# Kernel optimization log

Hardware: AMD Instinct MI355X
Metric: run time of the kernel (lower is better)

Reference implementation:

```python
import jax, jax.numpy as jnp
import numpy as np

B, DIM, L, H, W = 4, 128, 256, 8, 8
N = L * H * W
D_INNER, D_STATE, D_CONV, DT_RANK = 128, 8, 4, 8


def _ln(x, w, b, eps=1e-5):
    m = x.mean(-1, keepdims=True)
    v = ((x - m) ** 2).mean(-1, keepdims=True)
    return (x - m) * jax.lax.rsqrt(v + eps) * w + b


def _mamba_fusion(x, z_in, p, i):
    # x, z_in: (B, N, DIM). x drives the SSM; z_in provides the cross-modal gate.
    u = x @ p['Wx'][i]                                    # (B, N, D_INNER)
    z = z_in @ p['Wz'][i]                                 # (B, N, D_INNER)
    # causal depthwise conv1d along tokens, kernel D_CONV (torch pad=k-1 then truncate)
    up = jnp.pad(u, ((0, 0), (D_CONV - 1, 0), (0, 0)))
    w = p['conv_w'][i]                                    # (D_INNER, D_CONV)
    uc = sum(up[:, k:k + u.shape[1], :] * w[:, k] for k in range(D_CONV)) + p['conv_b'][i]
    uc = jax.nn.silu(uc)
    x_dbl = uc @ p['Wxproj'][i]                           # (B, N, DT_RANK + 2*D_STATE)
    dt_r, Bm, Cm = jnp.split(x_dbl, [DT_RANK, DT_RANK + D_STATE], axis=-1)
    dt = jax.nn.softplus(dt_r @ p['Wdt'][i] + p['bdt'][i])  # (B, N, D_INNER)
    A = -jnp.exp(p['A_log'][i])                           # (D_INNER, D_STATE)
    dA = jnp.exp(dt[..., None] * A)                       # (B, N, D_INNER, D_STATE)
    dBu = dt[..., None] * Bm[:, :, None, :] * uc[..., None]

    def step(h, inp):
        dA_t, dBu_t, C_t = inp
        h = dA_t * h + dBu_t                              # (B, D_INNER, D_STATE)
        return h, jnp.einsum('bds,bs->bd', h, C_t)

    h0 = jnp.zeros((u.shape[0], D_INNER, D_STATE), u.dtype)
    _, ys = jax.lax.scan(step, h0, (dA.swapaxes(0, 1), dBu.swapaxes(0, 1), Cm.swapaxes(0, 1)))
    y = ys.swapaxes(0, 1) + p['Dp'][i] * uc
    y = y * jax.nn.silu(z)
    return y @ p['Wout_m'][i] + p['bout_m'][i]


def _cross_block(in0, in1, p, i):
    skip = in0
    a = _ln(in0, p['ln0_w'][i], p['ln0_b'][i])
    b = _ln(in1, p['ln1_w'][i], p['ln1_b'][i])
    return skip + _mamba_fusion(a, b, p, i)


def setup_inputs() -> dict:
    key = jax.random.key(0)
    ks = jax.random.split(key, 16)
    s_in = 1.0 / np.sqrt(DIM)
    s_di = 1.0 / np.sqrt(D_INNER)
    inp = {
        'front': jax.random.normal(ks[0], (B, DIM, L, H, W), jnp.float32),
        'back': jax.random.normal(ks[1], (B, DIM, L, H, W), jnp.float32),
        'ln0_w': jnp.ones((2, DIM), jnp.float32),
        'ln0_b': jnp.zeros((2, DIM), jnp.float32),
        'ln1_w': jnp.ones((2, DIM), jnp.float32),
        'ln1_b': jnp.zeros((2, DIM), jnp.float32),
        'Wx': jax.random.normal(ks[2], (2, DIM, D_INNER), jnp.float32) * s_in,
        'Wz': jax.random.normal(ks[3], (2, DIM, D_INNER), jnp.float32) * s_in,
        'conv_w': jax.random.normal(ks[4], (2, D_INNER, D_CONV), jnp.float32) * 0.5,
        'conv_b': jnp.zeros((2, D_INNER), jnp.float32),
        'Wxproj': jax.random.normal(ks[5], (2, D_INNER, DT_RANK + 2 * D_STATE), jnp.float32) * s_di,
        'Wdt': jax.random.normal(ks[6], (2, DT_RANK, D_INNER), jnp.float32) * (1.0 / np.sqrt(DT_RANK)),
        'bdt': jnp.full((2, D_INNER), -4.6, jnp.float32),  # softplus^-1(~0.01)
        'A_log': jnp.broadcast_to(jnp.log(jnp.arange(1, D_STATE + 1, dtype=jnp.float32)), (2, D_INNER, D_STATE)).copy(),
        'Dp': jnp.ones((2, D_INNER), jnp.float32),
        'Wout_m': jax.random.normal(ks[7], (2, D_INNER, DIM), jnp.float32) * s_di,
        'bout_m': jnp.zeros((2, DIM), jnp.float32),
        'Wout': jax.random.normal(ks[8], (DIM, DIM), jnp.float32) * s_in,
        'bout': jnp.zeros((DIM,), jnp.float32),
    }
    return inp


def reference(front, back, ln0_w, ln0_b, ln1_w, ln1_b, Wx, Wz, conv_w, conv_b,
              Wxproj, Wdt, bdt, A_log, Dp, Wout_m, bout_m, Wout, bout):
    p = dict(ln0_w=ln0_w, ln0_b=ln0_b, ln1_w=ln1_w, ln1_b=ln1_b, Wx=Wx, Wz=Wz,
             conv_w=conv_w, conv_b=conv_b, Wxproj=Wxproj, Wdt=Wdt, bdt=bdt,
             A_log=A_log, Dp=Dp, Wout_m=Wout_m, bout_m=bout_m)
    ff = front.reshape(B, DIM, N).swapaxes(1, 2)          # (B, N, DIM)
    bf = back.reshape(B, DIM, N).swapaxes(1, 2)
    f_fus = _cross_block(ff, bf, p, 0)
    b_fus = _cross_block(bf, ff, p, 1)
    fusion = ((f_fus + b_fus) * 0.5) @ Wout + bout
    return fusion.swapaxes(1, 2).reshape(B, DIM, L, H, W)
```

## Files before the change

### kernel.cpp

```cpp
#include <hip/hip_runtime.h>

#define DEV static __device__ __forceinline__

typedef short s16x8 __attribute__((ext_vector_type(8)));
typedef float f32x4 __attribute__((ext_vector_type(4)));
typedef unsigned short u16;
typedef unsigned int u32;

DEV float b2f(u16 u){ return __uint_as_float(((unsigned int)u) << 16); }
DEV u16 f2b(float f){
  unsigned int x = __float_as_uint(f);
  x += 0x7fffu + ((x >> 16) & 1u);
  return (u16)(x >> 16);
}
DEV float silu_f(float x){ return x * __builtin_amdgcn_rcpf(1.f + __expf(-x)); }
DEV float softplus_f(float x){ return (x > 15.f) ? x : __logf(1.f + __expf(x)); }
DEV bool detf32(const void* lnw){ return *(const unsigned int*)lnw == 0x3F800000u; }
DEV float ldin(const void* p, long long i, bool f){
  return f ? ((const float*)p)[i] : b2f(((const u16*)p)[i]);
}

static constexpr int BATCH = 4;
static constexpr int NSEQ  = 16384;
static constexpr int RTOT  = BATCH * NSEQ;
static constexpr int GCH   = 256;
static constexpr int DIRSZ = BATCH*GCH*128*8;

DEV int swz(int row, int col){ return (row << 7) + (col ^ ((row & 7) << 3)); }

__global__ __launch_bounds__(256) void k_setup(
                        const void* ln0w, const void* ln0b, const void* ln1w, const void* ln1b,
                        const void* Wx, const void* Wz, const void* Wxp, const void* Wdt,
                        const void* bdt, const void* Alog, const void* convw, const void* convb,
                        const void* Dpr, const void* Woutm, const void* boutm,
                        const void* Wout, const void* bout,
                        u16* Wuz, u16* WdtBC, u16* Wcat, u16* WoutT,
                        float* buz, float* bdtf, float* bcat, float* boutf,
                        float* Aexp, float* convwF, float* convbF, float* DpF)
{
  bool f = detf32(ln0w);
  int tid = blockIdx.x * 256 + threadIdx.x;
  int gs  = gridDim.x * 256;
  for (int idx = tid; idx < 2*256*128; idx += gs){
    int d = idx >> 15; int n = (idx >> 7) & 255; int k = idx & 127;
    float wv;
    if (n < 128) wv = ldin(ln0w, d*128+k, f) * ldin(Wx, (long long)(d*128+k)*128 + n, f);
    else         wv = ldin(ln1w, (1-d)*128+k, f) * ldin(Wz, (long long)((1-d)*128+k)*128 + (n-128), f);
    Wuz[idx] = f2b(wv);
  }
  for (int idx = tid; idx < 2*256; idx += gs){
    int d = idx >> 8; int n = idx & 255;
    float s = 0.f;
    if (n < 128){
      for (int k = 0; k < 128; ++k)
        s += ldin(ln0b, d*128+k, f) * ldin(Wx, (long long)(d*128+k)*128 + n, f);
    } else {
      for (int k = 0; k < 128; ++k)
        s += ldin(ln1b, (1-d)*128+k, f) * ldin(Wz, (long long)((1-d)*128+k)*128 + (n-128), f);
    }
    buz[idx] = s;
  }
  for (int idx = tid; idx < 2*128; idx += gs)
    bdtf[idx] = ldin(bdt, idx, f);
  for (int idx = tid; idx < 2*144*128; idx += gs){
    int i = idx / (144*128); int rem = idx % (144*128); int n = rem >> 7; int k = rem & 127;
    if (n < 128){
      float s = 0.f;
      for (int j = 0; j < 8; ++j)
        s += ldin(Wxp, (long long)(i*128+k)*24 + j, f) * ldin(Wdt, (long long)(i*8+j)*128 + n, f);
      WdtBC[idx] = f2b(s);
    } else {
      WdtBC[idx] = f2b(ldin(Wxp, (long long)(i*128+k)*24 + (n - 120), f));
    }
  }
  for (int idx = tid; idx < 128*256; idx += gs){
    int n = idx >> 8; int k = idx & 255;
    Wcat[idx] = f2b(ldin(Woutm, (long long)k*128 + n, f));
  }
  for (int idx = tid; idx < 128*128; idx += gs){
    int n = idx >> 7, k = idx & 127;
    WoutT[idx] = f2b(ldin(Wout, (long long)k*128 + n, f));
  }
  for (int idx = tid; idx < 128; idx += gs){
    bcat[idx]  = ldin(boutm, idx, f) + ldin(boutm, 128 + idx, f);
    boutf[idx] = ldin(bout, idx, f);
  }
  for (int idx = tid; idx < 2*128*8; idx += gs)
    Aexp[idx] = -expf(ldin(Alog, idx, f));
  for (int idx = tid; idx < 2*128*4; idx += gs)
    convwF[idx] = ldin(convw, idx, f);
  for (int idx = tid; idx < 2*128; idx += gs){
    convbF[idx] = ldin(convb, idx, f);
    DpF[idx]   = ldin(Dpr, idx, f);
  }
}

__global__ __launch_bounds__(256, 3) void k_lnguz(const void* front, const void* back,
                                                  const void* ln0w,
                                                  const u16* __restrict__ Wuz,
                                                  const float* __restrict__ buz,
                                                  u16* __restrict__ sfbh,
                                                  u16* __restrict__ u0, u16* __restrict__ u1,
                                                  u16* __restrict__ z0, u16* __restrict__ z1)
{
  bool fF = detf32(ln0w);
  __shared__ u16 Tf[64][130];
  __shared__ u16 Tb[64][130];
  __shared__ __align__(16) u16 Wl[64*128];
  __shared__ float Mf[64], Rf[64], Mb[64], Rb[64];
  int tid = threadIdx.x;
  long long r0 = (long long)blockIdx.x * 64;
  int b  = (int)(r0 >> 14);
  int n0 = (int)(r0 & 16383);
  if (fF){
    const float* fp = (const float*)front;
    const float* bp = (const float*)back;
    for (int it = 0; it < 8; ++it){
      int d = it*16 + (tid >> 4);
      int t = (tid & 15) * 4;
      long long gi = ((long long)(b*128 + d))*NSEQ + n0 + t;
      float4 vf = *(const float4*)&fp[gi];
      float4 vb = *(const float4*)&bp[gi];
      Tf[t+0][d] = f2b(vf.x); Tf[t+1][d] = f2b(vf.y);
      Tf[t+2][d] = f2b(vf.z); Tf[t+3][d] = f2b(vf.w);
      Tb[t+0][d] = f2b(vb.x); Tb[t+1][d] = f2b(vb.y);
      Tb[t+2][d] = f2b(vb.z); Tb[t+3][d] = f2b(vb.w);
    }
  } else {
    const u16* fp = (const u16*)front;
    const u16* bp = (const u16*)back;
    for (int it = 0; it < 4; ++it){
      int d = it*32 + (tid >> 3);
      int t = (tid & 7) * 8;
      long long gi = ((long long)(b*128 + d))*NSEQ + n0 + t;
      uint4 vf = *(const uint4*)&fp[gi];
      uint4 vb = *(const uint4*)&bp[gi];
      Tf[t+0][d] = (u16)vf.x; Tf[t+1][d] = (u16)(vf.x>>16);
      Tf[t+2][d] = (u16)vf.y; Tf[t+3][d] = (u16)(vf.y>>16);
      Tf[t+4][d] = (u16)vf.z; Tf[t+5][d] = (u16)(vf.z>>16);
      Tf[t+6][d] = (u16)vf.w; Tf[t+7][d] = (u16)(vf.w>>16);
      Tb[t+0][d] = (u16)vb.x; Tb[t+1][d] = (u16)(vb.x>>16);
      Tb[t+2][d] = (u16)vb.y; Tb[t+3][d] = (u16)(vb.y>>16);
      Tb[t+4][d] = (u16)vb.z; Tb[t+5][d] = (u16)(vb.z>>16);
      Tb[t+6][d] = (u16)vb.w; Tb[t+7][d] = (u16)(vb.w>>16);
    }
  }
  __syncthreads();
  {
    int t = tid >> 2, sub = tid & 3;
    float s = 0.f, ss = 0.f, s2 = 0.f, ss2 = 0.f;
    for (int k = 0; k < 32; ++k){
      float v = b2f(Tf[t][sub*32 + k]); s  += v; ss  += v*v;
      float w = b2f(Tb[t][sub*32 + k]); s2 += w; ss2 += w*w;
    }
    for (int m = 1; m < 4; m <<= 1){
      s  += __shfl_xor(s,  m, 64); ss  += __shfl_xor(ss,  m, 64);
      s2 += __shfl_xor(s2, m, 64); ss2 += __shfl_xor(ss2, m, 64);
    }
    if (sub == 0){
      float mf = s  * (1.f/128.f); float vf = ss  * (1.f/128.f) - mf*mf;
      Mf[t] = mf; Rf[t] = rsqrtf(vf + 1e-5f);
      float mb = s2 * (1.f/128.f); float vb = ss2 * (1.f/128.f) - mb*mb;
      Mb[t] = mb; Rb[t] = rsqrtf(vb + 1e-5f);
    }
  }
  __syncthreads();
  for (int it = 0; it < 8; ++it){
    int t = it*8 + (tid >> 5);
    int c = (tid & 31) * 4;
    float mf = Mf[t], rf = Rf[t], mb = Mb[t], rb = Rb[t];
    float f0 = b2f(Tf[t][c+0]), f1 = b2f(Tf[t][c+1]), f2 = b2f(Tf[t][c+2]), f3 = b2f(Tf[t][c+3]);
    float g0 = b2f(Tb[t][c+0]), g1 = b2f(Tb[t][c+1]), g2 = b2f(Tb[t][c+2]), g3 = b2f(Tb[t][c+3]);
    ushort4 so;
    so.x = f2b(f0+g0); so.y = f2b(f1+g1); so.z = f2b(f2+g2); so.w = f2b(f3+g3);
    *(ushort4*)&sfbh[(r0 + t)*128 + c] = so;
    Tf[t][c+0] = f2b((f0-mf)*rf); Tf[t][c+1] = f2b((f1-mf)*rf);
    Tf[t][c+2] = f2b((f2-mf)*rf); Tf[t][c+3] = f2b((f3-mf)*rf);
    Tb[t][c+0] = f2b((g0-mb)*rb); Tb[t][c+1] = f2b((g1-mb)*rb);
    Tb[t][c+2] = f2b((g2-mb)*rb); Tb[t][c+3] = f2b((g3-mb)*rb);
  }
  __syncthreads();
  int w = tid >> 6, lane = tid & 63;
  int q = lane >> 4, m = lane & 15;
  for (int dir = 0; dir < 2; ++dir){
    const u16* At = dir ? &Tb[0][0] : &Tf[0][0];
    const u16* Wt = Wuz + dir*256*128;
    const float* bias = buz + dir*256;
    u16* outU = dir ? u1 : u0;
    u16* outZ = dir ? z0 : z1;
    for (int ch = 0; ch < 4; ++ch){
      for (int ci = tid; ci < 64*16; ci += 256){
        int n = ci >> 4, c8 = ci & 15;
        *(uint4*)&Wl[(n << 7) + ((c8 ^ (n & 7)) << 3)] = *(const uint4*)&Wt[(ch*64 + n)*128 + c8*8];
      }
      __syncthreads();
      f32x4 acc[4];
      #pragma unroll
      for (int ct = 0; ct < 4; ++ct) acc[ct] = (f32x4){0.f,0.f,0.f,0.f};
      #pragma unroll
      for (int kt = 0; kt < 4; ++kt){
        const u16* ap = At + (w*16 + m)*130 + kt*32 + q*8;
        union { u32 w4[4]; s16x8 v; } au;
        au.w4[0] = *(const u32*)&ap[0];
        au.w4[1] = *(const u32*)&ap[2];
        au.w4[2] = *(const u32*)&ap[4];
        au.w4[3] = *(const u32*)&ap[6];
        int sc = (kt*32 + q*8) ^ ((m & 7) << 3);
        #pragma unroll
        for (int ct = 0; ct < 4; ++ct){
          s16x8 bf = *(const s16x8*)&Wl[((ct*16 + m) << 7) + sc];
          acc[ct] = __builtin_amdgcn_mfma_f32_16x16x32_bf16(au.v, bf, acc[ct], 0, 0, 0);
        }
      }
      #pragma unroll
      for (int ct = 0; ct < 4; ++ct){
        int col = ch*64 + ct*16 + m;
        #pragma unroll
        for (int i = 0; i < 4; ++i){
          long long r = r0 + w*16 + q*4 + i;
          float v = acc[ct][i] + bias[col];
          if (col < 128) outU[r*128 + col] = f2b(v);
          else           outZ[r*128 + (col - 128)] = f2b(silu_f(v));
        }
      }
      __syncthreads();
    }
  }
}

__global__ __launch_bounds__(256, 3) void k_cps(const u16* __restrict__ u0p,
                                             const u16* __restrict__ u1p,
                                             const float* __restrict__ convwF,
                                             const float* __restrict__ convbF,
                                             const u16* __restrict__ WdtBC,
                                             const float* __restrict__ bdtf,
                                             const float* __restrict__ Aexp,
                                             u16* __restrict__ uc0p, u16* __restrict__ uc1p,
                                             u16* __restrict__ yg,
                                             float* __restrict__ BCg,
                                             float* __restrict__ P, float* __restrict__ Q)
{
  __shared__ __align__(16) u16 AlF[64*128];
  __shared__ __align__(16) u16 WlF[144*128];
  int dir = blockIdx.y;
  const u16* u = dir ? u1p : u0p;
  u16* ucb = dir ? uc1p : uc0p;
  const u16* Wt = WdtBC + dir*18432;
  const float* bias = bdtf + dir*128;
  u16* dtb = yg + dir*128;
  float* BC = BCg + (long long)dir*RTOT*16;
  int tid = threadIdx.x;
  long long r0 = (long long)blockIdx.x * 64;
  int b  = (int)(r0 >> 14);
  int n0 = (int)(r0 & 16383);
  for (int ci = tid; ci < 144*16; ci += 256){
    int n = ci >> 4, c8 = ci & 15;
    *(uint4*)&WlF[(n << 7) + ((c8 ^ (n & 7)) << 3)] = *(const uint4*)&Wt[n*128 + c8*8];
  }
  {
    int c = tid & 127, h = tid >> 7;
    const float* wp = &convwF[(dir*128 + c)*4];
    float w0 = wp[0], w1 = wp[1], w2 = wp[2], w3 = wp[3];
    float cb = convbF[dir*128 + c];
    int t0 = h*32;
    const u16* up = u + (long long)b*NSEQ*128 + c;
    int nbase = n0 + t0;
    float win0 = (nbase-3 >= 0) ? b2f(up[(long long)(nbase-3)*128]) : 0.f;
    float win1 = (nbase-2 >= 0) ? b2f(up[(long long)(nbase-2)*128]) : 0.f;
    float win2 = (nbase-1 >= 0) ? b2f(up[(long long)(nbase-1)*128]) : 0.f;
    #pragma unroll
    for (int t = 0; t < 32; ++t){
      float cur = b2f(up[(long long)(nbase + t)*128]);
      float a = win0*w0 + win1*w1 + win2*w2 + cur*w3 + cb;
      u16 s = f2b(silu_f(a));
      AlF[swz(t0 + t, c)] = s;
      ucb[(r0 + t0 + t)*128 + c] = s;
      win0 = win1; win1 = win2; win2 = cur;
    }
  }
  __syncthreads();
  int w = tid >> 6, lane = tid & 63;
  int q = lane >> 4, m = lane & 15;
  f32x4 acc[9];
  #pragma unroll
  for (int ct = 0; ct < 9; ++ct) acc[ct] = (f32x4){0.f,0.f,0.f,0.f};
  #pragma unroll
  for (int kt = 0; kt < 4; ++kt){
    int sc = (kt*32 + q*8) ^ ((m & 7) << 3);
    s16x8 af = *(const s16x8*)&AlF[((w*16 + m) << 7) + sc];
    #pragma unroll
    for (int ct = 0; ct < 9; ++ct){
      s16x8 bf = *(const s16x8*)&WlF[((ct*16 + m) << 7) + sc];
      acc[ct] = __builtin_amdgcn_mfma_f32_16x16x32_bf16(af, bf, acc[ct], 0, 0, 0);
    }
  }
  __syncthreads();
  u16* Dl = WlF;
  float* BCl = (float*)&WlF[64*128];
  #pragma unroll
  for (int ct = 0; ct < 9; ++ct){
    int col = ct*16 + m;
    #pragma unroll
    for (int i = 0; i < 4; ++i){
      int rl = w*16 + q*4 + i;
      long long r = r0 + rl;
      float v = acc[ct][i];
      if (col < 128){
        u16 dv = f2b(softplus_f(v + bias[col]));
        dtb[r*256 + col] = dv;
        Dl[swz(rl, col)] = dv;
      } else {
        BC[r*16 + (col - 128)] = v;
        BCl[rl*16 + (col - 128)] = v;
      }
    }
  }
  __syncthreads();
  {
    int c = tid & 127, sh = tid >> 7;
    int g = (int)(r0 & 16383) >> 6;
    int base = sh*4;
    float Ac[4], Pr[4], H[4];
    bool fast = true;
    #pragma unroll
    for (int j = 0; j < 4; ++j){
      Ac[j] = Aexp[(dir*128 + c)*8 + base + j];
      fast = fast && (fabsf(Ac[j] + (float)(base + j + 1)) < 2e-4f);
      H[j] = 0.f;
    }
    float sd = 0.f;
    if (fast){
      if (sh == 0){
        for (int t = 0; t < 64; ++t){
          int ce = swz(t, c);
          float d  = b2f(Dl[ce]);
          float uu = b2f(AlF[ce]);
          float du = d * uu;
          sd += d;
          float E  = __expf(-d);
          float E2 = E*E, E3 = E2*E, E4 = E2*E2;
          float4 bc = *(const float4*)&BCl[t*16];
          H[0] = E *H[0] + du*bc.x;
          H[1] = E2*H[1] + du*bc.y;
          H[2] = E3*H[2] + du*bc.z;
          H[3] = E4*H[3] + du*bc.w;
        }
        float Es = __expf(-sd);
        Pr[0] = Es; Pr[1] = Es*Es; Pr[2] = Pr[1]*Es; Pr[3] = Pr[1]*Pr[1];
      } else {
        for (int t = 0; t < 64; ++t){
          int ce = swz(t, c);
          float d  = b2f(Dl[ce]);
          float uu = b2f(AlF[ce]);
          float du = d * uu;
          sd += d;
          float E  = __expf(-d);
          float E2 = E*E, E4 = E2*E2;
          float E5 = E4*E, E6 = E5*E, E7 = E6*E, E8 = E7*E;
          float4 bc = *(const float4*)&BCl[t*16 + 4];
          H[0] = E5*H[0] + du*bc.x;
          H[1] = E6*H[1] + du*bc.y;
          H[2] = E7*H[2] + du*bc.z;
          H[3] = E8*H[3] + du*bc.w;
        }
        float Es = __expf(-sd);
        float Es2 = Es*Es, Es4 = Es2*Es2;
        Pr[0] = Es4*Es; Pr[1] = Es4*Es2; Pr[2] = Pr[1]*Es; Pr[3] = Es4*Es4;
      }
    } else {
      for (int t = 0; t < 64; ++t){
        int ce = swz(t, c);
        float d  = b2f(Dl[ce]);
        float uu = b2f(AlF[ce]);
        float du = d * uu;
        sd += d;
        #pragma unroll
        for (int j = 0; j < 4; ++j){
          float dA = __expf(d * Ac[j]);
          H[j]  = dA*H[j] + du*BCl[t*16 + base + j];
        }
      }
      #pragma unroll
      for (int j = 0; j < 4; ++j) Pr[j] = __expf(sd * Ac[j]);
    }
    long long o = (long long)dir*DIRSZ + (((long long)b*GCH + g)*128 + c)*8 + base;
    *(float4*)&P[o] = make_float4(Pr[0],Pr[1],Pr[2],Pr[3]);
    *(float4*)&Q[o] = make_float4(H[0],H[1],H[2],H[3]);
  }
}

__global__ __launch_bounds__(64) void k_scan2(const float* __restrict__ P,
                                              const float* __restrict__ Q,
                                              float* __restrict__ hinit)
{
  int idx = blockIdx.x*64 + threadIdx.x;
  int dir = idx >> 12;
  int rem = idx & 4095;
  int b  = rem >> 10;
  int cs = rem & 1023;
  long long base = (long long)dir*DIRSZ + (long long)b*GCH*1024 + cs;
  float h = 0.f;
  for (int g = 0; g < GCH; g += 8){
    long long o = base + (long long)g*1024;
    float p[8], qv[8];
    #pragma unroll
    for (int j = 0; j < 8; ++j){ p[j] = P[o + j*1024]; qv[j] = Q[o + j*1024]; }
    #pragma unroll
    for (int j = 0; j < 8; ++j){
      hinit[o + j*1024] = h;
      h = p[j]*h + qv[j];
    }
  }
}

__global__ __launch_bounds__(256) void k_scan3(const u16* __restrict__ uc0p,
                                               const u16* __restrict__ uc1p,
                                               const float* __restrict__ BCg,
                                               const float* __restrict__ hinit,
                                               const u16* __restrict__ z0p,
                                               const u16* __restrict__ z1p,
                                               const float* __restrict__ DpF,
                                               const float* __restrict__ Aexp,
                                               u16* yg)
{
  __shared__ float Bl[128][8];
  __shared__ float Cl[128][8];
  int dir = blockIdx.y;
  const u16* uc = dir ? uc1p : uc0p;
  const u16* zs = dir ? z1p : z0p;
  const float* BC = BCg + (long long)dir*RTOT*16;
  int tid = threadIdx.x;
  int gp = blockIdx.x & 127;
  int b  = blockIdx.x >> 7;
  long long tokbase = (long long)b*NSEQ + gp*128;
  for (int idx = tid; idx < 128*8; idx += 256){
    int row = idx >> 3, s = idx & 7;
    Bl[row][s] = BC[(tokbase + row)*16 + s];
    Cl[row][s] = BC[(tokbase + row)*16 + 8 + s];
  }
  __syncthreads();
  int c = tid & 127;
  int gh = tid >> 7;
  int g = gp*2 + gh;
  int doff = dir*128;
  float Ac[8], H[8];
  long long ho = (long long)dir*DIRSZ + (((long long)b*GCH + g)*128 + c)*8;
  float4 h0 = *(const float4*)&hinit[ho];
  float4 h1 = *(const float4*)&hinit[ho + 4];
  H[0]=h0.x; H[1]=h0.y; H[2]=h0.z; H[3]=h0.w;
  H[4]=h1.x; H[5]=h1.y; H[6]=h1.z; H[7]=h1.w;
  bool fast = true;
  #pragma unroll
  for (int s = 0; s < 8; ++s){
    Ac[s] = Aexp[(dir*128 + c)*8 + s];
    fast = fast && (fabsf(Ac[s] + (float)(s + 1)) < 2e-4f);
  }
  float dpc = DpF[dir*128 + c];
  long long rbase = (long long)b*NSEQ + g*64;
  if (fast){
    for (int t = 0; t < 64; ++t){
      long long r = rbase + t;
      float d  = b2f(yg[r*256 + doff + c]);
      float uu = b2f(uc[r*128 + c]);
      float du = d * uu;
      int rowl = gh*64 + t;
      float E  = __expf(-d);
      float E2 = E*E, E3 = E2*E, E4 = E2*E2;
      float dA[8] = {E, E2, E3, E4, E4*E, E4*E2, E4*E3, E4*E4};
      float y = 0.f;
      #pragma unroll
      for (int s = 0; s < 8; ++s){
        H[s] = dA[s]*H[s] + du*Bl[rowl][s];
        y += H[s]*Cl[rowl][s];
      }
      float zv = b2f(zs[r*128 + c]);
      yg[r*256 + doff + c] = f2b((y + dpc*uu) * zv);
    }
  } else {
    for (int t = 0; t < 64; ++t){
      long long r = rbase + t;
      float d  = b2f(yg[r*256 + doff + c]);
      float uu = b2f(uc[r*128 + c]);
      float du = d * uu;
      int rowl = gh*64 + t;
      float y = 0.f;
      #pragma unroll
      for (int s = 0; s < 8; ++s){
        float dA = __expf(d * Ac[s]);
        H[s] = dA*H[s] + du*Bl[rowl][s];
        y += H[s]*Cl[rowl][s];
      }
      float zv = b2f(zs[r*128 + c]);
      yg[r*256 + doff + c] = f2b((y + dpc*uu) * zv);
    }
  }
}

__global__ __launch_bounds__(256, 3) void k_tail(const u16* __restrict__ yg,
                                              const u16* __restrict__ Wcat,
                                              const float* __restrict__ bcat,
                                              const u16* __restrict__ sfbh,
                                              const u16* __restrict__ WoutT,
                                              const float* __restrict__ boutf,
                                              void* outp, const void* dflag)
{
  __shared__ u16 Wl[128][136];
  __shared__ u16 Al[64][136];
  int tid = threadIdx.x;
  long long r0 = (long long)blockIdx.x * 64;
  int w = tid >> 6, lane = tid & 63;
  int q = lane >> 4, m = lane & 15;
  f32x4 acc[8];
  #pragma unroll
  for (int ct = 0; ct < 8; ++ct) acc[ct] = (f32x4){0.f,0.f,0.f,0.f};
  for (int kp = 0; kp < 2; ++kp){
    if (kp) __syncthreads();
    for (int ci = tid; ci < 128*16; ci += 256){
      int n = ci >> 4, c8 = ci & 15;
      *(uint4*)&Wl[n][c8*8] = *(const uint4*)&Wcat[n*256 + kp*128 + c8*8];
    }
    for (int ci = tid; ci < 64*16; ci += 256){
      int rl = ci >> 4, c8 = ci & 15;
      *(uint4*)&Al[rl][c8*8] = *(const uint4*)&yg[(r0 + rl)*256 + kp*128 + c8*8];
    }
    __syncthreads();
    #pragma unroll
    for (int kt = 0; kt < 4; ++kt){
      s16x8 af = *(const s16x8*)&Al[w*16 + m][kt*32 + q*8];
      #pragma unroll
      for (int ct = 0; ct < 8; ++ct){
        s16x8 bf = *(const s16x8*)&Wl[ct*16 + m][kt*32 + q*8];
        acc[ct] = __builtin_amdgcn_mfma_f32_16x16x32_bf16(af, bf, acc[ct], 0, 0, 0);
      }
    }
  }
  __syncthreads();
  #pragma unroll
  for (int ct = 0; ct < 8; ++ct){
    int col = ct*16 + m;
    #pragma unroll
    for (int i = 0; i < 4; ++i){
      int rl = w*16 + q*4 + i;
      long long r = r0 + rl;
      Al[rl][col] = f2b(acc[ct][i] + bcat[col] + b2f(sfbh[r*128 + col]));
    }
  }
  for (int ci = tid; ci < 128*16; ci += 256){
    int n = ci >> 4, c8 = ci & 15;
    *(uint4*)&Wl[n][c8*8] = *(const uint4*)&WoutT[n*128 + c8*8];
  }
  __syncthreads();
  f32x4 acc2[8];
  #pragma unroll
  for (int ct = 0; ct < 8; ++ct) acc2[ct] = (f32x4){0.f,0.f,0.f,0.f};
  #pragma unroll
  for (int kt = 0; kt < 4; ++kt){
    s16x8 af = *(const s16x8*)&Al[w*16 + m][kt*32 + q*8];
    #pragma unroll
    for (int ct = 0; ct < 8; ++ct){
      s16x8 bf = *(const s16x8*)&Wl[ct*16 + m][kt*32 + q*8];
      acc2[ct] = __builtin_amdgcn_mfma_f32_16x16x32_bf16(af, bf, acc2[ct], 0, 0, 0);
    }
  }
  __syncthreads();
  u16* Tl = &Wl[0][0];
  #pragma unroll
  for (int ct = 0; ct < 8; ++ct){
    int col = ct*16 + m;
    #pragma unroll
    for (int i = 0; i < 4; ++i){
      int rl = w*16 + q*4 + i;
      Tl[col*68 + rl] = f2b(0.5f*acc2[ct][i] + boutf[col]);
    }
  }
  __syncthreads();
  long long b = r0 >> 14; long long tok0 = r0 & 16383;
  bool fo = detf32(dflag);
  if (fo){
    float* of = (float*)outp;
    for (int idx = tid; idx < 128*16; idx += 256){
      int n = idx >> 4; int t0 = (idx & 15)*4;
      float4 v;
      v.x = b2f(Tl[n*68 + t0+0]); v.y = b2f(Tl[n*68 + t0+1]);
      v.z = b2f(Tl[n*68 + t0+2]); v.w = b2f(Tl[n*68 + t0+3]);
      *(float4*)&of[(((long long)(b*128 + n)) << 14) + tok0 + t0] = v;
    }
  } else {
    u16* ob = (u16*)outp;
    for (int idx = tid; idx < 128*16; idx += 256){
      int n = idx >> 4; int t0 = (idx & 15)*4;
      ushort4 v;
      v.x = Tl[n*68 + t0+0]; v.y = Tl[n*68 + t0+1];
      v.z = Tl[n*68 + t0+2]; v.w = Tl[n*68 + t0+3];
      *(ushort4*)&ob[(((long long)(b*128 + n)) << 14) + tok0 + t0] = v;
    }
  }
}

extern "C" void kernel_launch(void* const* d_in, const int* in_sizes, int n_in,
                              void* d_out, int out_size, void* d_ws, size_t ws_size,
                              hipStream_t stream)
{
  (void)in_sizes; (void)n_in; (void)out_size; (void)ws_size;
  const void* front = d_in[0];
  const void* back  = d_in[1];
  const void* ln0w  = d_in[2];
  const void* ln0b  = d_in[3];
  const void* ln1w  = d_in[4];
  const void* ln1b  = d_in[5];
  const void* Wx    = d_in[6];
  const void* Wz    = d_in[7];
  const void* convw = d_in[8];
  const void* convb = d_in[9];
  const void* Wxp   = d_in[10];
  const void* Wdt   = d_in[11];
  const void* bdt   = d_in[12];
  const void* Alog  = d_in[13];
  const void* Dpr   = d_in[14];
  const void* Woutm = d_in[15];
  const void* boutm = d_in[16];
  const void* Wout  = d_in[17];
  const void* bout  = d_in[18];

  char* p = (char*)d_ws;
  auto alloc = [&](size_t bytes) -> void* {
    void* q = (void*)p; p += (bytes + 255) & ~(size_t)255; return q;
  };
  u16*   uc0   = (u16*)  alloc((size_t)RTOT*128*2);
  u16*   uc1   = (u16*)  alloc((size_t)RTOT*128*2);
  u16*   sfbh  = (u16*)  alloc((size_t)RTOT*128*2);
  u16*   u0    = (u16*)  alloc((size_t)RTOT*128*2);
  u16*   u1    = (u16*)  alloc((size_t)RTOT*128*2);
  u16*   z0    = (u16*)  alloc((size_t)RTOT*128*2);
  u16*   z1    = (u16*)  alloc((size_t)RTOT*128*2);
  float* BC    = (float*)alloc((size_t)2*RTOT*16*4);
  float* Pb    = (float*)alloc((size_t)2*DIRSZ*4);
  float* Qb    = (float*)alloc((size_t)2*DIRSZ*4);
  float* hin   = (float*)alloc((size_t)2*DIRSZ*4);
  u16*   yg    = (u16*)  alloc((size_t)RTOT*256*2);
  u16*   Wuz   = (u16*)  alloc(2*256*128*2);
  u16*   WdtBC = (u16*)  alloc(2*144*128*2);
  u16*   Wcat  = (u16*)  alloc(128*256*2);
  u16*   WoutT = (u16*)  alloc(128*128*2);
  float* buz   = (float*)alloc(2*256*4);
  float* bdtf  = (float*)alloc(2*128*4);
  float* bcat  = (float*)alloc(128*4);
  float* boutf = (float*)alloc(128*4);
  float* Aexp  = (float*)alloc(2*128*8*4);
  float* convwF= (float*)alloc(2*128*4*4);
  float* convbF= (float*)alloc(2*128*4);
  float* DpF   = (float*)alloc(2*128*4);

  k_setup<<<128,256,0,stream>>>(ln0w,ln0b,ln1w,ln1b,Wx,Wz,Wxp,Wdt,bdt,Alog,convw,convb,Dpr,
                                Woutm,boutm,Wout,bout,
                                Wuz,WdtBC,Wcat,WoutT,buz,bdtf,bcat,boutf,Aexp,
                                convwF,convbF,DpF);
  k_lnguz<<<RTOT/64,256,0,stream>>>(front, back, ln0w, Wuz, buz, sfbh,
                                    u0, u1, z0, z1);
  dim3 g2(RTOT/64, 2);
  k_cps<<<g2,256,0,stream>>>(u0, u1, convwF, convbF, WdtBC, bdtf, Aexp,
                             uc0, uc1, yg, BC, Pb, Qb);
  k_scan2<<<128,64,0,stream>>>(Pb, Qb, hin);
  dim3 g3(BATCH*GCH/2, 2);
  k_scan3<<<g3,256,0,stream>>>(uc0, uc1, BC, hin, z0, z1, DpF, Aexp, yg);
  k_tail<<<RTOT/64,256,0,stream>>>(yg, Wcat, bcat, sfbh, WoutT, boutf, d_out, ln0w);
}
```

Measured before the change: 312.1 us.

## Register-prefetch weight tiles to overlap global loads with MFMA in GEMM kernels

In the LN+projection kernel and the tail kernel, the next weight (and activation) tile is now loaded from global memory into registers before the current tile's MFMA work runs, so load latency overlaps with compute. The LN kernel also hoists the A-fragment loads out of the chunk loop and drops one barrier per iteration. The scan kernel batches eight timesteps' global loads ahead of the recurrence so memory latency is less serialized. This costs more registers per thread, which may reduce occupancy under the launch bounds.

Result: slower. 359.8 us (+15.3%).

```diff
diff --git a/kernel.cpp b/kernel.cpp
--- a/kernel.cpp
+++ b/kernel.cpp
@@ -112,6 +112,7 @@
   long long r0 = (long long)blockIdx.x * 64;
   int b  = (int)(r0 >> 14);
   int n0 = (int)(r0 & 16383);
+  int pn = tid >> 4, pc8 = tid & 15;
   if (fF){
     const float* fp = (const float*)front;
     const float* bp = (const float*)back;
@@ -145,6 +146,10 @@
       Tb[t+6][d] = (u16)vb.w; Tb[t+7][d] = (u16)(vb.w>>16);
     }
   }
+  uint4 wreg[4];
+  #pragma unroll
+  for (int k = 0; k < 4; ++k)
+    wreg[k] = *(const uint4*)&Wuz[(pn + 16*k)*128 + pc8*8];
   __syncthreads();
   {
     int t = tid >> 2, sub = tid & 3;
@@ -182,21 +187,22 @@
   __syncthreads();
   int w = tid >> 6, lane = tid & 63;
   int q = lane >> 4, m = lane & 15;
-  for (int dir = 0; dir < 2; ++dir){
-    const u16* At = dir ? &Tb[0][0] : &Tf[0][0];
-    const u16* Wt = Wuz + dir*256*128;
-    const float* bias = buz + dir*256;
-    u16* outU = dir ? u1 : u0;
-    u16* outZ = dir ? z0 : z1;
-    for (int ch = 0; ch < 4; ++ch){
-      for (int ci = tid; ci < 64*16; ci += 256){
-        int n = ci >> 4, c8 = ci & 15;
-        *(uint4*)&Wl[(n << 7) + ((c8 ^ (n & 7)) << 3)] = *(const uint4*)&Wt[(ch*64 + n)*128 + c8*8];
-      }
-      __syncthreads();
-      f32x4 acc[4];
+  s16x8 afr[4];
+  for (int rd = 0; rd < 8; ++rd){
+    int dir = rd >> 2;
+    #pragma unroll
+    for (int k = 0; k < 4; ++k)
+      *(uint4*)&Wl[((pn + 16*k) << 7) + ((pc8 ^ (pn & 7)) << 3)] = wreg[k];
+    __syncthreads();
+    if (rd < 7){
+      int nd = (rd+1) >> 2, nc = (rd+1) & 3;
+      const u16* Wt = Wuz + nd*256*128;
       #pragma unroll
-      for (int ct = 0; ct < 4; ++ct) acc[ct] = (f32x4){0.f,0.f,0.f,0.f};
+      for (int k = 0; k < 4; ++k)
+        wreg[k] = *(const uint4*)&Wt[(nc*64 + pn + 16*k)*128 + pc8*8];
+    }
+    if ((rd & 3) == 0){
+      const u16* At = dir ? &Tb[0][0] : &Tf[0][0];
       #pragma unroll
       for (int kt = 0; kt < 4; ++kt){
         const u16* ap = At + (w*16 + m)*130 + kt*32 + q*8;
@@ -205,13 +211,26 @@
         au.w4[1] = *(const u32*)&ap[2];
         au.w4[2] = *(const u32*)&ap[4];
         au.w4[3] = *(const u32*)&ap[6];
-        int sc = (kt*32 + q*8) ^ ((m & 7) << 3);
-        #pragma unroll
-        for (int ct = 0; ct < 4; ++ct){
-          s16x8 bf = *(const s16x8*)&Wl[((ct*16 + m) << 7) + sc];
-          acc[ct] = __builtin_amdgcn_mfma_f32_16x16x32_bf16(au.v, bf, acc[ct], 0, 0, 0);
-        }
-      }
+        afr[kt] = au.v;
+      }
+    }
+    f32x4 acc[4];
+    #pragma unroll
+    for (int ct = 0; ct < 4; ++ct) acc[ct] = (f32x4){0.f,0.f,0.f,0.f};
+    #pragma unroll
+    for (int kt = 0; kt < 4; ++kt){
+      int sc = (kt*32 + q*8) ^ ((m & 7) << 3);
+      #pragma unroll
+      for (int ct = 0; ct < 4; ++ct){
+        s16x8 bf = *(const s16x8*)&Wl[((ct*16 + m) << 7) + sc];
+        acc[ct] = __builtin_amdgcn_mfma_f32_16x16x32_bf16(afr[kt], bf, acc[ct], 0, 0, 0);
+      }
+    }
+    {
+      int ch = rd & 3;
+      const float* bias = buz + dir*256;
+      u16* outU = dir ? u1 : u0;
+      u16* outZ = dir ? z0 : z1;
       #pragma unroll
       for (int ct = 0; ct < 4; ++ct){
         int col = ch*64 + ct*16 + m;
@@ -223,8 +242,8 @@
           else           outZ[r*128 + (col - 128)] = f2b(silu_f(v));
         }
       }
-      __syncthreads();
-    }
+    }
+    if (rd < 7) __syncthreads();
   }
 }
 
@@ -458,23 +477,31 @@
   float dpc = DpF[dir*128 + c];
   long long rbase = (long long)b*NSEQ + g*64;
   if (fast){
-    for (int t = 0; t < 64; ++t){
-      long long r = rbase + t;
-      float d  = b2f(yg[r*256 + doff + c]);
-      float uu = b2f(uc[r*128 + c]);
-      float du = d * uu;
-      int rowl = gh*64 + t;
-      float E  = __expf(-d);
-      float E2 = E*E, E3 = E2*E, E4 = E2*E2;
-      float dA[8] = {E, E2, E3, E4, E4*E, E4*E2, E4*E3, E4*E4};
-      float y = 0.f;
+    for (int t0 = 0; t0 < 64; t0 += 8){
+      float dv[8], uv[8], zvv[8];
       #pragma unroll
-      for (int s = 0; s < 8; ++s){
-        H[s] = dA[s]*H[s] + du*Bl[rowl][s];
-        y += H[s]*Cl[rowl][s];
-      }
-      float zv = b2f(zs[r*128 + c]);
-      yg[r*256 + doff + c] = f2b((y + dpc*uu) * zv);
+      for (int j = 0; j < 8; ++j){
+        long long r = rbase + t0 + j;
+        dv[j]  = b2f(yg[r*256 + doff + c]);
+        uv[j]  = b2f(uc[r*128 + c]);
+        zvv[j] = b2f(zs[r*128 + c]);
+      }
+      #pragma unroll
+      for (int j = 0; j < 8; ++j){
+        float d = dv[j], uu = uv[j];
+        float du = d * uu;
+        int rowl = gh*64 + t0 + j;
+        float E  = __expf(-d);
+        float E2 = E*E, E3 = E2*E, E4 = E2*E2;
+        float dA[8] = {E, E2, E3, E4, E4*E, E4*E2, E4*E3, E4*E4};
+        float y = 0.f;
+        #pragma unroll
+        for (int s = 0; s < 8; ++s){
+          H[s] = dA[s]*H[s] + du*Bl[rowl][s];
+          y += H[s]*Cl[rowl][s];
+        }
+        yg[(rbase + t0 + j)*256 + doff + c] = f2b((y + dpc*uu) * zvv[j]);
+      }
     }
   } else {
     for (int t = 0; t < 64; ++t){
@@ -510,28 +537,53 @@
   long long r0 = (long long)blockIdx.x * 64;
   int w = tid >> 6, lane = tid & 63;
   int q = lane >> 4, m = lane & 15;
+  int sn = tid >> 4, sc8 = tid & 15;
+  uint4 wreg[8], areg[4];
+  #pragma unroll
+  for (int k = 0; k < 8; ++k)
+    wreg[k] = *(const uint4*)&Wcat[(sn + 16*k)*256 + sc8*8];
+  #pragma unroll
+  for (int k = 0; k < 4; ++k)
+    areg[k] = *(const uint4*)&yg[(r0 + sn + 16*k)*256 + sc8*8];
+  #pragma unroll
+  for (int k = 0; k < 8; ++k) *(uint4*)&Wl[sn + 16*k][sc8*8] = wreg[k];
+  #pragma unroll
+  for (int k = 0; k < 4; ++k) *(uint4*)&Al[sn + 16*k][sc8*8] = areg[k];
+  __syncthreads();
+  #pragma unroll
+  for (int k = 0; k < 8; ++k)
+    wreg[k] = *(const uint4*)&Wcat[(sn + 16*k)*256 + 128 + sc8*8];
+  #pragma unroll
+  for (int k = 0; k < 4; ++k)
+    areg[k] = *(const uint4*)&yg[(r0 + sn + 16*k)*256 + 128 + sc8*8];
   f32x4 acc[8];
   #pragma unroll
   for (int ct = 0; ct < 8; ++ct) acc[ct] = (f32x4){0.f,0.f,0.f,0.f};
-  for (int kp = 0; kp < 2; ++kp){
-    if (kp) __syncthreads();
-    for (int ci = tid; ci < 128*16; ci += 256){
-      int n = ci >> 4, c8 = ci & 15;
-      *(uint4*)&Wl[n][c8*8] = *(const uint4*)&Wcat[n*256 + kp*128 + c8*8];
-    }
-    for (int ci = tid; ci < 64*16; ci += 256){
-      int rl = ci >> 4, c8 = ci & 15;
-      *(uint4*)&Al[rl][c8*8] = *(const uint4*)&yg[(r0 + rl)*256 + kp*128 + c8*8];
-    }
-    __syncthreads();
-    #pragma unroll
-    for (int kt = 0; kt < 4; ++kt){
-      s16x8 af = *(const s16x8*)&Al[w*16 + m][kt*32 + q*8];
-      #pragma unroll
-      for (int ct = 0; ct < 8; ++ct){
-        s16x8 bf = *(const s16x8*)&Wl[ct*16 + m][kt*32 + q*8];
-        acc[ct] = __builtin_amdgcn_mfma_f32_16x16x32_bf16(af, bf, acc[ct], 0, 0, 0);
-      }
+  #pragma unroll
+  for (int kt = 0; kt < 4; ++kt){
+    s16x8 af = *(const s16x8*)&Al[w*16 + m][kt*32 + q*8];
+    #pragma unroll
+    for (int ct = 0; ct < 8; ++ct){
+      s16x8 bf = *(const s16x8*)&Wl[ct*16 + m][kt*32 + q*8];
+      acc[ct] = __builtin_amdgcn_mfma_f32_16x16x32_bf16(af, bf, acc[ct], 0, 0, 0);
+    }
+  }
+  __syncthreads();
+  #pragma unroll
+  for (int k = 0; k < 8; ++k) *(uint4*)&Wl[sn + 16*k][sc8*8] = wreg[k];
+  #pragma unroll
+  for (int k = 0; k < 4; ++k) *(uint4*)&Al[sn + 16*k][sc8*8] = areg[k];
+  __syncthreads();
+  #pragma unroll
+  for (int k = 0; k < 8; ++k)
+    wreg[k] = *(const uint4*)&WoutT[(sn + 16*k)*128 + sc8*8];
+  #pragma unroll
+  for (int kt = 0; kt < 4; ++kt){
+    s16x8 af = *(const s16x8*)&Al[w*16 + m][kt*32 + q*8];
+    #pragma unroll
+    for (int ct = 0; ct < 8; ++ct){
+      s16x8 bf = *(const s16x8*)&Wl[ct*16 + m][kt*32 + q*8];
+      acc[ct] = __builtin_amdgcn_mfma_f32_16x16x32_bf16(af, bf, acc[ct], 0, 0, 0);
     }
   }
   __syncthreads();
@@ -545,10 +597,9 @@
       Al[rl][col] = f2b(acc[ct][i] + bcat[col] + b2f(sfbh[r*128 + col]));
     }
   }
-  for (int ci = tid; ci < 128*16; ci += 256){
-    int n = ci >> 4, c8 = ci & 15;
-    *(uint4*)&Wl[n][c8*8] = *(const uint4*)&WoutT[n*128 + c8*8];
-  }
+  #pragma unroll
+  for (int k = 0; k < 8; ++k)
+    *(uint4*)&Wl[sn + 16*k][sc8*8] = wreg[k];
   __syncthreads();
   f32x4 acc2[8];
   #pragma unroll
```

## Split scan chunks into halves with mid-chunk carry to double scan3 parallelism

Applied to the files above, without the earlier changes.

k_cps now also records the partial decay product and state after the first 32 tokens of each 64-token chunk (Pa/Qa). k_scan3 launches one block per chunk instead of per chunk pair, and each half-block rebuilds its starting state from hinit combined with Pa/Qa, so the sequential inner loop drops from 64 to 32 steps. The aim is to shorten the serial recurrence and raise occupancy in the final scan. In exchange it adds two extra float buffers to write and read, plus a small amount of extra work in k_cps.

Result: no change. 317.2 us (+1.6%).

```diff
diff --git a/kernel.cpp b/kernel.cpp
--- a/kernel.cpp
+++ b/kernel.cpp
@@ -238,7 +238,8 @@
                                              u16* __restrict__ uc0p, u16* __restrict__ uc1p,
                                              u16* __restrict__ yg,
                                              float* __restrict__ BCg,
-                                             float* __restrict__ P, float* __restrict__ Q)
+                                             float* __restrict__ P, float* __restrict__ Q,
+                                             float* __restrict__ Pa, float* __restrict__ Qa)
 {
   __shared__ __align__(16) u16 AlF[64*128];
   __shared__ __align__(16) u16 WlF[144*128];
@@ -321,6 +322,8 @@
     int g = (int)(r0 & 16383) >> 6;
     int base = sh*4;
     float Ac[4], Pr[4], H[4];
+    float Pa0=1.f, Pa1=1.f, Pa2=1.f, Pa3=1.f;
+    float Qa0=0.f, Qa1=0.f, Qa2=0.f, Qa3=0.f;
     bool fast = true;
     #pragma unroll
     for (int j = 0; j < 4; ++j){
@@ -331,61 +334,85 @@
     float sd = 0.f;
     if (fast){
       if (sh == 0){
-        for (int t = 0; t < 64; ++t){
+        for (int half = 0; half < 2; ++half){
+          for (int t = half*32; t < half*32 + 32; ++t){
+            int ce = swz(t, c);
+            float d  = b2f(Dl[ce]);
+            float uu = b2f(AlF[ce]);
+            float du = d * uu;
+            sd += d;
+            float E  = __expf(-d);
+            float E2 = E*E, E3 = E2*E, E4 = E2*E2;
+            float4 bc = *(const float4*)&BCl[t*16];
+            H[0] = E *H[0] + du*bc.x;
+            H[1] = E2*H[1] + du*bc.y;
+            H[2] = E3*H[2] + du*bc.z;
+            H[3] = E4*H[3] + du*bc.w;
+          }
+          if (half == 0){
+            float Es = __expf(-sd);
+            Pa0 = Es; Pa1 = Es*Es; Pa2 = Pa1*Es; Pa3 = Pa1*Pa1;
+            Qa0 = H[0]; Qa1 = H[1]; Qa2 = H[2]; Qa3 = H[3];
+          }
+        }
+        float Es = __expf(-sd);
+        Pr[0] = Es; Pr[1] = Es*Es; Pr[2] = Pr[1]*Es; Pr[3] = Pr[1]*Pr[1];
+      } else {
+        for (int half = 0; half < 2; ++half){
+          for (int t = half*32; t < half*32 + 32; ++t){
+            int ce = swz(t, c);
+            float d  = b2f(Dl[ce]);
+            float uu = b2f(AlF[ce]);
+            float du = d * uu;
+            sd += d;
+            float E  = __expf(-d);
+            float E2 = E*E, E4 = E2*E2;
+            float E5 = E4*E, E6 = E5*E, E7 = E6*E, E8 = E7*E;
+            float4 bc = *(const float4*)&BCl[t*16 + 4];
+            H[0] = E5*H[0] + du*bc.x;
+            H[1] = E6*H[1] + du*bc.y;
+            H[2] = E7*H[2] + du*bc.z;
+            H[3] = E8*H[3] + du*bc.w;
+          }
+          if (half == 0){
+            float Es = __expf(-sd);
+            float Es2 = Es*Es, Es4 = Es2*Es2;
+            Pa0 = Es4*Es; Pa1 = Es4*Es2; Pa2 = Pa1*Es; Pa3 = Es4*Es4;
+            Qa0 = H[0]; Qa1 = H[1]; Qa2 = H[2]; Qa3 = H[3];
+          }
+        }
+        float Es = __expf(-sd);
+        float Es2 = Es*Es, Es4 = Es2*Es2;
+        Pr[0] = Es4*Es; Pr[1] = Es4*Es2; Pr[2] = Pr[1]*Es; Pr[3] = Es4*Es4;
+      }
+    } else {
+      for (int half = 0; half < 2; ++half){
+        for (int t = half*32; t < half*32 + 32; ++t){
           int ce = swz(t, c);
           float d  = b2f(Dl[ce]);
           float uu = b2f(AlF[ce]);
           float du = d * uu;
           sd += d;
-          float E  = __expf(-d);
-          float E2 = E*E, E3 = E2*E, E4 = E2*E2;
-          float4 bc = *(const float4*)&BCl[t*16];
-          H[0] = E *H[0] + du*bc.x;
-          H[1] = E2*H[1] + du*bc.y;
-          H[2] = E3*H[2] + du*bc.z;
-          H[3] = E4*H[3] + du*bc.w;
+          #pragma unroll
+          for (int j = 0; j < 4; ++j){
+            float dA = __expf(d * Ac[j]);
+            H[j]  = dA*H[j] + du*BCl[t*16 + base + j];
+          }
         }
-        float Es = __expf(-sd);
-        Pr[0] = Es; Pr[1] = Es*Es; Pr[2] = Pr[1]*Es; Pr[3] = Pr[1]*Pr[1];
-      } else {
-        for (int t = 0; t < 64; ++t){
-          int ce = swz(t, c);
-          float d  = b2f(Dl[ce]);
-          float uu = b2f(AlF[ce]);
-          float du = d * uu;
-          sd += d;
-          float E  = __expf(-d);
-          float E2 = E*E, E4 = E2*E2;
-          float E5 = E4*E, E6 = E5*E, E7 = E6*E, E8 = E7*E;
-          float4 bc = *(const float4*)&BCl[t*16 + 4];
-          H[0] = E5*H[0] + du*bc.x;
-          H[1] = E6*H[1] + du*bc.y;
-          H[2] = E7*H[2] + du*bc.z;
-          H[3] = E8*H[3] + du*bc.w;
-        }
-        float Es = __expf(-sd);
-        float Es2 = Es*Es, Es4 = Es2*Es2;
-        Pr[0] = Es4*Es; Pr[1] = Es4*Es2; Pr[2] = Pr[1]*Es; Pr[3] = Es4*Es4;
-      }
-    } else {
-      for (int t = 0; t < 64; ++t){
-        int ce = swz(t, c);
-        float d  = b2f(Dl[ce]);
-        float uu = b2f(AlF[ce]);
-        float du = d * uu;
-        sd += d;
-        #pragma unroll
-        for (int j = 0; j < 4; ++j){
-          float dA = __expf(d * Ac[j]);
-          H[j]  = dA*H[j] + du*BCl[t*16 + base + j];
+        if (half == 0){
+          Pa0 = __expf(sd*Ac[0]); Pa1 = __expf(sd*Ac[1]);
+          Pa2 = __expf(sd*Ac[2]); Pa3 = __expf(sd*Ac[3]);
+          Qa0 = H[0]; Qa1 = H[1]; Qa2 = H[2]; Qa3 = H[3];
         }
       }
       #pragma unroll
       for (int j = 0; j < 4; ++j) Pr[j] = __expf(sd * Ac[j]);
     }
     long long o = (long long)dir*DIRSZ + (((long long)b*GCH + g)*128 + c)*8 + base;
-    *(float4*)&P[o] = make_float4(Pr[0],Pr[1],Pr[2],Pr[3]);
-    *(float4*)&Q[o] = make_float4(H[0],H[1],H[2],H[3]);
+    *(float4*)&P[o]  = make_float4(Pr[0],Pr[1],Pr[2],Pr[3]);
+    *(float4*)&Q[o]  = make_float4(H[0],H[1],H[2],H[3]);
+    *(float4*)&Pa[o] = make_float4(Pa0,Pa1,Pa2,Pa3);
+    *(float4*)&Qa[o] = make_float4(Qa0,Qa1,Qa2,Qa3);
   }
 }
 
@@ -417,38 +444,52 @@
                                                const u16* __restrict__ uc1p,
                                                const float* __restrict__ BCg,
                                                const float* __restrict__ hinit,
+                                               const float* __restrict__ Pa,
+                                               const float* __restrict__ Qa,
                                                const u16* __restrict__ z0p,
                                                const u16* __restrict__ z1p,
                                                const float* __restrict__ DpF,
                                                const float* __restrict__ Aexp,
                                                u16* yg)
 {
-  __shared__ float Bl[128][8];
-  __shared__ float Cl[128][8];
+  __shared__ float Bl[64][8];
+  __shared__ float Cl[64][8];
   int dir = blockIdx.y;
   const u16* uc = dir ? uc1p : uc0p;
   const u16* zs = dir ? z1p : z0p;
   const float* BC = BCg + (long long)dir*RTOT*16;
   int tid = threadIdx.x;
-  int gp = blockIdx.x & 127;
-  int b  = blockIdx.x >> 7;
-  long long tokbase = (long long)b*NSEQ + gp*128;
-  for (int idx = tid; idx < 128*8; idx += 256){
+  int g  = blockIdx.x;
+  int b  = g >> 8;
+  int gl = g & 255;
+  long long tokbase = (long long)b*NSEQ + gl*64;
+  for (int idx = tid; idx < 64*8; idx += 256){
     int row = idx >> 3, s = idx & 7;
     Bl[row][s] = BC[(tokbase + row)*16 + s];
     Cl[row][s] = BC[(tokbase + row)*16 + 8 + s];
   }
   __syncthreads();
-  int c = tid & 127;
-  int gh = tid >> 7;
-  int g = gp*2 + gh;
+  int c   = tid & 127;
+  int sub = tid >> 7;
   int doff = dir*128;
   float Ac[8], H[8];
-  long long ho = (long long)dir*DIRSZ + (((long long)b*GCH + g)*128 + c)*8;
-  float4 h0 = *(const float4*)&hinit[ho];
-  float4 h1 = *(const float4*)&hinit[ho + 4];
-  H[0]=h0.x; H[1]=h0.y; H[2]=h0.z; H[3]=h0.w;
-  H[4]=h1.x; H[5]=h1.y; H[6]=h1.z; H[7]=h1.w;
+  long long ho = (long long)dir*DIRSZ + (((long long)b*GCH + gl)*128 + c)*8;
+  {
+    float4 h0 = *(const float4*)&hinit[ho];
+    float4 h1 = *(const float4*)&hinit[ho + 4];
+    H[0]=h0.x; H[1]=h0.y; H[2]=h0.z; H[3]=h0.w;
+    H[4]=h1.x; H[5]=h1.y; H[6]=h1.z; H[7]=h1.w;
+  }
+  if (sub){
+    float4 pa0 = *(const float4*)&Pa[ho];
+    float4 pa1 = *(const float4*)&Pa[ho + 4];
+    float4 qa0 = *(const float4*)&Qa[ho];
+    float4 qa1 = *(const float4*)&Qa[ho + 4];
+    H[0] = pa0.x*H[0] + qa0.x; H[1] = pa0.y*H[1] + qa0.y;
+    H[2] = pa0.z*H[2] + qa0.z; H[3] = pa0.w*H[3] + qa0.w;
+    H[4] = pa1.x*H[4] + qa1.x; H[5] = pa1.y*H[5] + qa1.y;
+    H[6] = pa1.z*H[6] + qa1.z; H[7] = pa1.w*H[7] + qa1.w;
+  }
   bool fast = true;
   #pragma unroll
   for (int s = 0; s < 8; ++s){
@@ -456,14 +497,15 @@
     fast = fast && (fabsf(Ac[s] + (float)(s + 1)) < 2e-4f);
   }
   float dpc = DpF[dir*128 + c];
-  long long rbase = (long long)b*NSEQ + g*64;
+  long long rbase = tokbase + sub*32;
+  int rowb = sub*32;
   if (fast){
-    for (int t = 0; t < 64; ++t){
+    for (int t = 0; t < 32; ++t){
       long long r = rbase + t;
       float d  = b2f(yg[r*256 + doff + c]);
       float uu = b2f(uc[r*128 + c]);
       float du = d * uu;
-      int rowl = gh*64 + t;
+      int rowl = rowb + t;
       float E  = __expf(-d);
       float E2 = E*E, E3 = E2*E, E4 = E2*E2;
       float dA[8] = {E, E2, E3, E4, E4*E, E4*E2, E4*E3, E4*E4};
@@ -477,12 +519,12 @@
       yg[r*256 + doff + c] = f2b((y + dpc*uu) * zv);
     }
   } else {
-    for (int t = 0; t < 64; ++t){
+    for (int t = 0; t < 32; ++t){
       long long r = rbase + t;
       float d  = b2f(yg[r*256 + doff + c]);
       float uu = b2f(uc[r*128 + c]);
       float du = d * uu;
-      int rowl = gh*64 + t;
+      int rowl = rowb + t;
       float y = 0.f;
       #pragma unroll
       for (int s = 0; s < 8; ++s){
@@ -637,6 +679,8 @@
   float* Pb    = (float*)alloc((size_t)2*DIRSZ*4);
   float* Qb    = (float*)alloc((size_t)2*DIRSZ*4);
   float* hin   = (float*)alloc((size_t)2*DIRSZ*4);
+  float* PaB   = (float*)alloc((size_t)2*DIRSZ*4);
+  float* QaB   = (float*)alloc((size_t)2*DIRSZ*4);
   u16*   yg    = (u16*)  alloc((size_t)RTOT*256*2);
   u16*   Wuz   = (u16*)  alloc(2*256*128*2);
   u16*   WdtBC = (u16*)  alloc(2*144*128*2);
@@ -659,9 +703,9 @@
                                     u0, u1, z0, z1);
   dim3 g2(RTOT/64, 2);
   k_cps<<<g2,256,0,stream>>>(u0, u1, convwF, convbF, WdtBC, bdtf, Aexp,
-                             uc0, uc1, yg, BC, Pb, Qb);
+                             uc0, uc1, yg, BC, Pb, Qb, PaB, QaB);
   k_scan2<<<128,64,0,stream>>>(Pb, Qb, hin);
-  dim3 g3(BATCH*GCH/2, 2);
-  k_scan3<<<g3,256,0,stream>>>(uc0, uc1, BC, hin, z0, z1, DpF, Aexp, yg);
+  dim3 g3(BATCH*GCH, 2);
+  k_scan3<<<g3,256,0,stream>>>(uc0, uc1, BC, hin, PaB, QaB, z0, z1, DpF, Aexp, yg);
   k_tail<<<RTOT/64,256,0,stream>>>(yg, Wcat, bcat, sfbh, WoutT, boutf, d_out, ln0w);
 }
```
